# Kernel tuning notes

Hardware: AMD Instinct MI355X
Metric: run time of the kernel (lower is better)

Reference implementation:

```python
import jax, jax.numpy as jnp
import numpy as np

B, S, D = 16, 2048, 768
DOWNS = [16, 32, 64, 128]


def setup_inputs() -> dict:
    key = jax.random.key(0)
    ks = jax.random.split(key, 2 + 4 * len(DOWNS))
    inp = {
        "x": jax.random.normal(ks[0], (B, S, D), dtype=jnp.float32),
        "mask": jax.random.randint(ks[1], (B, S), 0, len(DOWNS), dtype=jnp.int64),
    }
    k = 2
    for i, ds in enumerate(DOWNS):
        inp[f"Wd{i}"] = jax.random.normal(ks[k], (D, ds), dtype=jnp.float32) * 0.02; k += 1
        inp[f"bd{i}"] = jax.random.normal(ks[k], (ds,), dtype=jnp.float32) * 0.02; k += 1
        inp[f"Wu{i}"] = jax.random.normal(ks[k], (ds, D), dtype=jnp.float32) * 0.02; k += 1
        inp[f"bu{i}"] = jax.random.normal(ks[k], (D,), dtype=jnp.float32) * 0.02; k += 1
    return inp


def reference(x, mask,
              Wd0, bd0, Wu0, bu0,
              Wd1, bd1, Wu1, bu1,
              Wd2, bd2, Wu2, bu2,
              Wd3, bd3, Wu3, bu3):
    # eval path, inference_level==0: all experts densely computed, then
    # per-token random mask selects one expert output (with residual) and sums.
    params = [(Wd0, bd0, Wu0, bu0), (Wd1, bd1, Wu1, bu1),
              (Wd2, bd2, Wu2, bu2), (Wd3, bd3, Wu3, bu3)]
    out = jnp.zeros_like(x)
    for i, (Wd, bd, Wu, bu) in enumerate(params):
        down = jax.nn.relu(jnp.einsum('bsd,dk->bsk', x, Wd) + bd)  # dropout is identity in eval
        up = jnp.einsum('bsk,kd->bsd', down, Wu) + bu + x          # residual add
        sel = (mask == i)[..., None].astype(x.dtype)               # [B,S,1]
        out = out + up * sel
    return out
```

## Files before the change

### kernel.cpp

```cpp
#include <hip/hip_runtime.h>
#include <hip/hip_bf16.h>

#define DIM 768
#define NTOK 32768
#define TTOK 16
#define NBLK 128

typedef __attribute__((ext_vector_type(8))) short short8;
typedef __attribute__((ext_vector_type(4))) float f32x4;

__device__ __forceinline__ unsigned short f2bf(float f) {
  union { float f; unsigned int u; } v; v.f = f;
  unsigned int u = v.u;
  return (unsigned short)((u + 0x7fffu + ((u >> 16) & 1u)) >> 16);
}
__device__ __forceinline__ float bf2f(unsigned short u) {
  union { unsigned int u; float f; } v; v.u = ((unsigned int)u) << 16; return v.f;
}

__global__ void hist_kernel(const int* __restrict__ mask, int* __restrict__ hist) {
  int tid = threadIdx.x, b = blockIdx.x;
  int gid = b * 256 + tid;
  int wv = tid >> 6, lane = tid & 63;
  int e = mask[gid] & 3;
  __shared__ int wcnt[4][4];
  #pragma unroll
  for (int q = 0; q < 4; ++q) {
    unsigned long long m = __ballot(e == q);
    if (lane == 0) wcnt[wv][q] = __popcll(m);
  }
  __syncthreads();
  if (tid < 4)
    hist[tid * NBLK + b] = wcnt[0][tid] + wcnt[1][tid] + wcnt[2][tid] + wcnt[3][tid];
}

__global__ void scan_kernel(const int* __restrict__ hist, int* __restrict__ base,
                            int* __restrict__ meta) {
  int lane = threadIdx.x;
  int v[8];
  int lsum = 0;
  #pragma unroll
  for (int j = 0; j < 8; ++j) {
    int t = hist[lane * 8 + j];
    v[j] = lsum; lsum += t;
  }
  int inc = lsum;
  #pragma unroll
  for (int d = 1; d < 64; d <<= 1) {
    int u = __shfl_up(inc, d);
    if (lane >= d) inc += u;
  }
  int excl = inc - lsum;
  #pragma unroll
  for (int j = 0; j < 8; ++j) base[lane * 8 + j] = excl + v[j];
  __syncthreads();
  if (lane == 0) {
    int est[5];
    #pragma unroll
    for (int e = 0; e < 4; ++e) est[e] = base[e * NBLK];
    est[4] = NTOK;
    #pragma unroll
    for (int e = 0; e < 5; ++e) meta[e] = est[e];
    int s = 0;
    #pragma unroll
    for (int e = 0; e < 4; ++e) {
      meta[8 + e] = s;
      s += (est[e + 1] - est[e] + TTOK - 1) / TTOK;
    }
    meta[12] = s;
    const int KPv[4] = {32, 32, 64, 128};
    int off = 0;
    #pragma unroll
    for (int e = 0; e < 4; ++e) {
      meta[16 + e] = off;
      int tiles = (est[e + 1] - est[e] + TTOK - 1) / TTOK;
      off += tiles * TTOK * KPv[e];
    }
  }
}

__global__ void scatter_kernel(const int* __restrict__ mask, const int* __restrict__ base,
                               int* __restrict__ lists) {
  int tid = threadIdx.x, b = blockIdx.x;
  int gid = b * 256 + tid;
  int wv = tid >> 6, lane = tid & 63;
  int e = mask[gid] & 3;
  __shared__ int wcnt[4][4];
  __shared__ int wbase[4][4];
  unsigned long long lt = (1ull << lane) - 1ull;
  int rank = 0;
  #pragma unroll
  for (int q = 0; q < 4; ++q) {
    unsigned long long m = __ballot(e == q);
    if (e == q) rank = __popcll(m & lt);
    if (lane == 0) wcnt[wv][q] = __popcll(m);
  }
  __syncthreads();
  if (tid < 4) {
    int s = 0;
    #pragma unroll
    for (int w2 = 0; w2 < 4; ++w2) { int c = wcnt[w2][tid]; wbase[w2][tid] = s; s += c; }
  }
  __syncthreads();
  lists[base[e * NBLK + b] + wbase[wv][e] + rank] = gid;
}

__global__ void prep_kernel(const float* __restrict__ Wd0, const float* __restrict__ Wd1,
                            const float* __restrict__ Wd2, const float* __restrict__ Wd3,
                            const float* __restrict__ Wu0, const float* __restrict__ Wu1,
                            const float* __restrict__ Wu2, const float* __restrict__ Wu3,
                            unsigned short* __restrict__ wdT, unsigned short* __restrict__ wuT) {
  int e = blockIdx.x;
  int ds = 16 << e;
  int lgK = (e == 0) ? 5 : (4 + e);
  int KP = 1 << lgK;
  const float* Wd = (e == 0) ? Wd0 : (e == 1) ? Wd1 : (e == 2) ? Wd2 : Wd3;
  const float* Wu = (e == 0) ? Wu0 : (e == 1) ? Wu1 : (e == 2) ? Wu2 : Wu3;
  const int WOFF[4] = {0, 12288, 36864, 86016};
  const int UOFF[4] = {0, 24576, 49152, 98304};
  int stride = gridDim.y * 256;
  int start = blockIdx.y * 256 + threadIdx.x;
  int nd = ds * DIM;
  for (int i = start; i < nd; i += stride) {
    int k = i / DIM, d = i - k * DIM;
    wdT[WOFF[e] + i] = f2bf(Wd[d * ds + k]);
  }
  int nu = DIM << lgK;
  for (int i = start; i < nu; i += stride) {
    int dc = i >> lgK, k = i & (KP - 1);
    wuT[UOFF[e] + i] = (k < ds) ? f2bf(Wu[k * DIM + dc]) : (unsigned short)0;
  }
}

__device__ __forceinline__ int expert_of(int w, const int* __restrict__ ts) {
  return (w >= ts[2]) ? ((w >= ts[3]) ? 3 : 2) : ((w >= ts[1]) ? 1 : 0);
}

template <int E>
__device__ __forceinline__ void down_tile(
    int wv, int lane, int tid, int tile, int cnt,
    const float* __restrict__ x, const int* __restrict__ listsE,
    const unsigned short* __restrict__ wd, const float* __restrict__ bd,
    unsigned short* __restrict__ dnE,
    unsigned short* __restrict__ xs, float* __restrict__ dnpart,
    unsigned short* __restrict__ dnt) {
  constexpr int DS = 16 << E;
  constexpr int KP = (E == 0) ? 32 : DS;
  constexpr int NTA = DS / 16;
  constexpr int SPLIT_N = (NTA < 4) ? NTA : 4;
  constexpr int SPLIT_K = 4 / SPLIT_N;
  constexpr int NTB = NTA / SPLIT_N;
  constexpr int KLEN = DIM / SPLIT_K;
  int base = tile * TTOK;
  int lrow = lane & 15, kg = lane >> 4;

  #pragma unroll
  for (int i = 0; i < 4; ++i) {
    int rr = base + wv * 4 + i;
    int t = (rr < cnt) ? listsE[rr] : -1;
    int r = wv * 4 + i;
    const float* src = x + (size_t)((t >= 0) ? t : 0) * DIM;
    #pragma unroll
    for (int j = 0; j < 3; ++j) {
      float4 v = {0.f, 0.f, 0.f, 0.f};
      if (t >= 0) v = *(const float4*)(src + j * 256 + lane * 4);
      ushort4 b;
      b.x = f2bf(v.x); b.y = f2bf(v.y); b.z = f2bf(v.z); b.w = f2bf(v.w);
      *(ushort4*)(xs + r * 776 + j * 256 + lane * 4) = b;
    }
  }
  if (SPLIT_K > 1) {
    for (int i = tid; i < TTOK * DS; i += 256) dnpart[i] = 0.f;
  }
  __syncthreads();

  int nsub = wv % SPLIT_N, ksub = wv / SPLIT_N;
  int d_base = ksub * KLEN;
  f32x4 acc[NTB];
  #pragma unroll
  for (int nb = 0; nb < NTB; ++nb) acc[nb] = f32x4{0.f, 0.f, 0.f, 0.f};

  for (int d0 = 0; d0 < KLEN; d0 += 64) {
    #pragma unroll
    for (int u = 0; u < 2; ++u) {
      int d = d_base + d0 + u * 32;
      short8 a = *(const short8*)(xs + lrow * 776 + d + kg * 8);
      #pragma unroll
      for (int nb = 0; nb < NTB; ++nb) {
        int n = nsub * NTB + nb;
        short8 b = *(const short8*)(wd + (size_t)(n * 16 + lrow) * DIM + d + kg * 8);
        acc[nb] = __builtin_amdgcn_mfma_f32_16x16x32_bf16(a, b, acc[nb], 0, 0, 0);
      }
    }
  }

  if (SPLIT_K > 1) {
    int kc = nsub * 16 + lrow;
    #pragma unroll
    for (int r = 0; r < 4; ++r)
      atomicAdd(&dnpart[(kg * 4 + r) * DS + kc], acc[0][r]);
    __syncthreads();
    for (int i = tid; i < TTOK * KP; i += 256) {
      int tt = i / KP, k = i - tt * KP;
      float v = (k < DS) ? fmaxf(dnpart[tt * DS + k] + bd[k], 0.f) : 0.f;
      dnt[tt * KP + k] = f2bf(v);
    }
  } else {
    #pragma unroll
    for (int nb = 0; nb < NTB; ++nb) {
      int kc = (nsub * NTB + nb) * 16 + lrow;
      float bv = bd[kc];
      #pragma unroll
      for (int r = 0; r < 4; ++r)
        dnt[(kg * 4 + r) * KP + kc] = f2bf(fmaxf(acc[nb][r] + bv, 0.f));
    }
  }
  __syncthreads();

  unsigned short* dst = dnE + (size_t)base * KP;
  constexpr int S = TTOK * KP;
  for (int i = tid * 8; i < S; i += 256 * 8)
    *(int4*)(dst + i) = *(const int4*)(dnt + i);
}

__global__ __launch_bounds__(256, 5) void down_main(
    const float* __restrict__ x,
    const int* __restrict__ meta, const int* __restrict__ lists,
    const unsigned short* __restrict__ wdT,
    const float* __restrict__ bd0, const float* __restrict__ bd1,
    const float* __restrict__ bd2, const float* __restrict__ bd3,
    unsigned short* __restrict__ dnc) {
  __shared__ unsigned short xs[TTOK * 776];
  __shared__ float dnpart[TTOK * 32];
  __shared__ unsigned short dnt[TTOK * 128];
  int tid = threadIdx.x, wv = tid >> 6, lane = tid & 63;
  const int* ts = meta + 8;
  int w = blockIdx.x;
  if (w >= ts[4]) return;
  int e = expert_of(w, ts);
  int tile = w - ts[e];
  int cnt = meta[e + 1] - meta[e];
  const int* listsE = lists + meta[e];
  const int WOFF[4] = {0, 12288, 36864, 86016};
  unsigned short* dnE = dnc + meta[16 + e];
  if (e == 0)
    down_tile<0>(wv, lane, tid, tile, cnt, x, listsE, wdT + WOFF[0], bd0, dnE, xs, dnpart, dnt);
  else if (e == 1)
    down_tile<1>(wv, lane, tid, tile, cnt, x, listsE, wdT + WOFF[1], bd1, dnE, xs, dnpart, dnt);
  else if (e == 2)
    down_tile<2>(wv, lane, tid, tile, cnt, x, listsE, wdT + WOFF[2], bd2, dnE, xs, dnpart, dnt);
  else
    down_tile<3>(wv, lane, tid, tile, cnt, x, listsE, wdT + WOFF[3], bd3, dnE, xs, dnpart, dnt);
}

template <int E>
__device__ __forceinline__ void up_tile(
    int wv, int lane, int tid, int tile, int cnt,
    const float* __restrict__ x, const int* __restrict__ listsE,
    const unsigned short* __restrict__ wu, const float* __restrict__ bu,
    const unsigned short* __restrict__ dnE, float* __restrict__ out,
    unsigned short* __restrict__ OL) {
  constexpr int DS = 16 << E;
  constexpr int KP = (E == 0) ? 32 : DS;
  constexpr int KB = KP / 32;
  int base = tile * TTOK;
  int lrow = lane & 15, kg = lane >> 4;

  short8 afr[KB];
  const unsigned short* dsrc = dnE + (size_t)(base + lrow) * KP + kg * 8;
  #pragma unroll
  for (int k = 0; k < KB; ++k) afr[k] = *(const short8*)(dsrc + k * 32);

  #pragma unroll 3
  for (int nn = 0; nn < 12; ++nn) {
    int n = wv * 12 + nn;
    f32x4 c = {0.f, 0.f, 0.f, 0.f};
    #pragma unroll
    for (int k = 0; k < KB; ++k) {
      short8 b = *(const short8*)(wu + (size_t)(n * 16 + lrow) * KP + k * 32 + kg * 8);
      c = __builtin_amdgcn_mfma_f32_16x16x32_bf16(afr[k], b, c, 0, 0, 0);
    }
    int dcol = n * 16 + lrow;
    float bv = bu[dcol];
    #pragma unroll
    for (int r = 0; r < 4; ++r)
      OL[(kg * 4 + r) * 772 + dcol] = f2bf(c[r] + bv);
  }
  __syncthreads();

  #pragma unroll
  for (int i = 0; i < 4; ++i) {
    int r = wv * 4 + i;
    int gr = base + r;
    int t = (gr < cnt) ? listsE[gr] : -1;
    if (t < 0) continue;
    const float* xsrc = x + (size_t)t * DIM;
    float* dst = out + (size_t)t * DIM;
    #pragma unroll
    for (int j = 0; j < 3; ++j) {
      int c4 = j * 256 + lane * 4;
      float4 xv = *(const float4*)(xsrc + c4);
      ushort4 ub = *(const ushort4*)(OL + r * 772 + c4);
      float4 o;
      o.x = xv.x + bf2f(ub.x);
      o.y = xv.y + bf2f(ub.y);
      o.z = xv.z + bf2f(ub.z);
      o.w = xv.w + bf2f(ub.w);
      *(float4*)(dst + c4) = o;
    }
  }
}

__global__ __launch_bounds__(256, 6) void up_main(
    const float* __restrict__ x,
    const int* __restrict__ meta, const int* __restrict__ lists,
    const unsigned short* __restrict__ wuT,
    const float* __restrict__ bu0, const float* __restrict__ bu1,
    const float* __restrict__ bu2, const float* __restrict__ bu3,
    const unsigned short* __restrict__ dnc, float* __restrict__ out) {
  __shared__ unsigned short OL[TTOK * 772];
  int tid = threadIdx.x, wv = tid >> 6, lane = tid & 63;
  const int* ts = meta + 8;
  int w = blockIdx.x;
  if (w >= ts[4]) return;
  int e = expert_of(w, ts);
  int tile = w - ts[e];
  int cnt = meta[e + 1] - meta[e];
  const int* listsE = lists + meta[e];
  const int UOFF[4] = {0, 24576, 49152, 98304};
  const unsigned short* dnE = dnc + meta[16 + e];
  if (e == 0)
    up_tile<0>(wv, lane, tid, tile, cnt, x, listsE, wuT + UOFF[0], bu0, dnE, out, OL);
  else if (e == 1)
    up_tile<1>(wv, lane, tid, tile, cnt, x, listsE, wuT + UOFF[1], bu1, dnE, out, OL);
  else if (e == 2)
    up_tile<2>(wv, lane, tid, tile, cnt, x, listsE, wuT + UOFF[2], bu2, dnE, out, OL);
  else
    up_tile<3>(wv, lane, tid, tile, cnt, x, listsE, wuT + UOFF[3], bu3, dnE, out, OL);
}

extern "C" void kernel_launch(void* const* d_in, const int* in_sizes, int n_in,
                              void* d_out, int out_size, void* d_ws, size_t ws_size,
                              hipStream_t stream) {
  const float* x = (const float*)d_in[0];
  const int* mask = (const int*)d_in[1];
  const float* Wd[4]; const float* bd[4]; const float* Wu[4]; const float* bu[4];
  for (int i = 0; i < 4; ++i) {
    Wd[i] = (const float*)d_in[2 + 4 * i];
    bd[i] = (const float*)d_in[3 + 4 * i];
    Wu[i] = (const float*)d_in[4 + 4 * i];
    bu[i] = (const float*)d_in[5 + 4 * i];
  }
  char* ws = (char*)d_ws;
  int* hist = (int*)ws;
  int* base = (int*)(ws + 2048);
  int* meta = (int*)(ws + 4096);
  int* lists = (int*)(ws + 4352);
  unsigned short* wdT = (unsigned short*)(ws + 135424);
  unsigned short* wuT = (unsigned short*)(ws + 504064);
  unsigned short* dnc = (unsigned short*)(ws + 897280);

  hist_kernel<<<NBLK, 256, 0, stream>>>(mask, hist);
  scan_kernel<<<1, 64, 0, stream>>>(hist, base, meta);
  scatter_kernel<<<NBLK, 256, 0, stream>>>(mask, base, lists);
  prep_kernel<<<dim3(4, 32), 256, 0, stream>>>(Wd[0], Wd[1], Wd[2], Wd[3],
                                               Wu[0], Wu[1], Wu[2], Wu[3], wdT, wuT);
  down_main<<<2051, 256, 0, stream>>>(x, meta, lists, wdT,
                                      bd[0], bd[1], bd[2], bd[3], dnc);
  up_main<<<2051, 256, 0, stream>>>(x, meta, lists, wuT,
                                    bu[0], bu[1], bu[2], bu[3], dnc,
                                    (float*)d_out);
}
```

Measured before the change: 116.0 us.

## Fuse down and up projections into persistent warp-specialized pipelined kernel

Replaces the separate down and up projection kernels with one persistent kernel of 512 blocks × 512 threads. Four waves gather x and run the down GEMM for tile i while the other four run the up GEMM and residual write for tile i-1, handing the intermediate activations through double-buffered shared memory. This removes the global round trip of the intermediate activations and one kernel launch, and overlaps the two stages. In exchange it adds extra block barriers per iteration, uses more LDS per block which may limit occupancy, and fixes the grid so some blocks may get one more tile than others.

Measured after the change: 100.8 us. -13.1%, faster.

```diff
diff --git a/kernel.cpp b/kernel.cpp
--- a/kernel.cpp
+++ b/kernel.cpp
@@ -5,6 +5,7 @@
 #define NTOK 32768
 #define TTOK 16
 #define NBLK 128
+#define GMAIN 512
 
 typedef __attribute__((ext_vector_type(8))) short short8;
 typedef __attribute__((ext_vector_type(4))) float f32x4;
@@ -68,14 +69,6 @@
       s += (est[e + 1] - est[e] + TTOK - 1) / TTOK;
     }
     meta[12] = s;
-    const int KPv[4] = {32, 32, 64, 128};
-    int off = 0;
-    #pragma unroll
-    for (int e = 0; e < 4; ++e) {
-      meta[16 + e] = off;
-      int tiles = (est[e + 1] - est[e] + TTOK - 1) / TTOK;
-      off += tiles * TTOK * KPv[e];
-    }
   }
 }
 
@@ -137,45 +130,21 @@
 }
 
 template <int E>
-__device__ __forceinline__ void down_tile(
-    int wv, int lane, int tid, int tile, int cnt,
-    const float* __restrict__ x, const int* __restrict__ listsE,
+__device__ __forceinline__ void down_g1(
+    int cwv, int lane,
     const unsigned short* __restrict__ wd, const float* __restrict__ bd,
-    unsigned short* __restrict__ dnE,
-    unsigned short* __restrict__ xs, float* __restrict__ dnpart,
-    unsigned short* __restrict__ dnt) {
+    const unsigned short* __restrict__ xs, float* __restrict__ dnpart,
+    unsigned short (*dnc)[136]) {
   constexpr int DS = 16 << E;
-  constexpr int KP = (E == 0) ? 32 : DS;
   constexpr int NTA = DS / 16;
   constexpr int SPLIT_N = (NTA < 4) ? NTA : 4;
   constexpr int SPLIT_K = 4 / SPLIT_N;
   constexpr int NTB = NTA / SPLIT_N;
   constexpr int KLEN = DIM / SPLIT_K;
-  int base = tile * TTOK;
   int lrow = lane & 15, kg = lane >> 4;
-
-  #pragma unroll
-  for (int i = 0; i < 4; ++i) {
-    int rr = base + wv * 4 + i;
-    int t = (rr < cnt) ? listsE[rr] : -1;
-    int r = wv * 4 + i;
-    const float* src = x + (size_t)((t >= 0) ? t : 0) * DIM;
-    #pragma unroll
-    for (int j = 0; j < 3; ++j) {
-      float4 v = {0.f, 0.f, 0.f, 0.f};
-      if (t >= 0) v = *(const float4*)(src + j * 256 + lane * 4);
-      ushort4 b;
-      b.x = f2bf(v.x); b.y = f2bf(v.y); b.z = f2bf(v.z); b.w = f2bf(v.w);
-      *(ushort4*)(xs + r * 776 + j * 256 + lane * 4) = b;
-    }
-  }
-  if (SPLIT_K > 1) {
-    for (int i = tid; i < TTOK * DS; i += 256) dnpart[i] = 0.f;
-  }
-  __syncthreads();
-
-  int nsub = wv % SPLIT_N, ksub = wv / SPLIT_N;
+  int nsub = cwv % SPLIT_N, ksub = cwv / SPLIT_N;
   int d_base = ksub * KLEN;
+
   f32x4 acc[NTB];
   #pragma unroll
   for (int nb = 0; nb < NTB; ++nb) acc[nb] = f32x4{0.f, 0.f, 0.f, 0.f};
@@ -199,12 +168,6 @@
     #pragma unroll
     for (int r = 0; r < 4; ++r)
       atomicAdd(&dnpart[(kg * 4 + r) * DS + kc], acc[0][r]);
-    __syncthreads();
-    for (int i = tid; i < TTOK * KP; i += 256) {
-      int tt = i / KP, k = i - tt * KP;
-      float v = (k < DS) ? fmaxf(dnpart[tt * DS + k] + bd[k], 0.f) : 0.f;
-      dnt[tt * KP + k] = f2bf(v);
-    }
   } else {
     #pragma unroll
     for (int nb = 0; nb < NTB; ++nb) {
@@ -212,68 +175,26 @@
       float bv = bd[kc];
       #pragma unroll
       for (int r = 0; r < 4; ++r)
-        dnt[(kg * 4 + r) * KP + kc] = f2bf(fmaxf(acc[nb][r] + bv, 0.f));
-    }
-  }
-  __syncthreads();
-
-  unsigned short* dst = dnE + (size_t)base * KP;
-  constexpr int S = TTOK * KP;
-  for (int i = tid * 8; i < S; i += 256 * 8)
-    *(int4*)(dst + i) = *(const int4*)(dnt + i);
-}
-
-__global__ __launch_bounds__(256, 5) void down_main(
-    const float* __restrict__ x,
-    const int* __restrict__ meta, const int* __restrict__ lists,
-    const unsigned short* __restrict__ wdT,
-    const float* __restrict__ bd0, const float* __restrict__ bd1,
-    const float* __restrict__ bd2, const float* __restrict__ bd3,
-    unsigned short* __restrict__ dnc) {
-  __shared__ unsigned short xs[TTOK * 776];
-  __shared__ float dnpart[TTOK * 32];
-  __shared__ unsigned short dnt[TTOK * 128];
-  int tid = threadIdx.x, wv = tid >> 6, lane = tid & 63;
-  const int* ts = meta + 8;
-  int w = blockIdx.x;
-  if (w >= ts[4]) return;
-  int e = expert_of(w, ts);
-  int tile = w - ts[e];
-  int cnt = meta[e + 1] - meta[e];
-  const int* listsE = lists + meta[e];
-  const int WOFF[4] = {0, 12288, 36864, 86016};
-  unsigned short* dnE = dnc + meta[16 + e];
-  if (e == 0)
-    down_tile<0>(wv, lane, tid, tile, cnt, x, listsE, wdT + WOFF[0], bd0, dnE, xs, dnpart, dnt);
-  else if (e == 1)
-    down_tile<1>(wv, lane, tid, tile, cnt, x, listsE, wdT + WOFF[1], bd1, dnE, xs, dnpart, dnt);
-  else if (e == 2)
-    down_tile<2>(wv, lane, tid, tile, cnt, x, listsE, wdT + WOFF[2], bd2, dnE, xs, dnpart, dnt);
-  else
-    down_tile<3>(wv, lane, tid, tile, cnt, x, listsE, wdT + WOFF[3], bd3, dnE, xs, dnpart, dnt);
+        dnc[kg * 4 + r][kc] = f2bf(fmaxf(acc[nb][r] + bv, 0.f));
+    }
+  }
 }
 
 template <int E>
-__device__ __forceinline__ void up_tile(
-    int wv, int lane, int tid, int tile, int cnt,
-    const float* __restrict__ x, const int* __restrict__ listsE,
+__device__ __forceinline__ void up_g2(
+    int cwv, int lane,
     const unsigned short* __restrict__ wu, const float* __restrict__ bu,
-    const unsigned short* __restrict__ dnE, float* __restrict__ out,
-    unsigned short* __restrict__ OL) {
-  constexpr int DS = 16 << E;
-  constexpr int KP = (E == 0) ? 32 : DS;
+    const unsigned short (*dnp)[136], unsigned short* __restrict__ OL) {
+  constexpr int KP = (E == 0) ? 32 : (16 << E);
   constexpr int KB = KP / 32;
-  int base = tile * TTOK;
   int lrow = lane & 15, kg = lane >> 4;
-
   short8 afr[KB];
-  const unsigned short* dsrc = dnE + (size_t)(base + lrow) * KP + kg * 8;
-  #pragma unroll
-  for (int k = 0; k < KB; ++k) afr[k] = *(const short8*)(dsrc + k * 32);
+  #pragma unroll
+  for (int k = 0; k < KB; ++k) afr[k] = *(const short8*)&dnp[lrow][k * 32 + kg * 8];
 
   #pragma unroll 3
   for (int nn = 0; nn < 12; ++nn) {
-    int n = wv * 12 + nn;
+    int n = cwv * 12 + nn;
     f32x4 c = {0.f, 0.f, 0.f, 0.f};
     #pragma unroll
     for (int k = 0; k < KB; ++k) {
@@ -286,57 +207,141 @@
     for (int r = 0; r < 4; ++r)
       OL[(kg * 4 + r) * 772 + dcol] = f2bf(c[r] + bv);
   }
-  __syncthreads();
-
-  #pragma unroll
-  for (int i = 0; i < 4; ++i) {
-    int r = wv * 4 + i;
-    int gr = base + r;
-    int t = (gr < cnt) ? listsE[gr] : -1;
-    if (t < 0) continue;
-    const float* xsrc = x + (size_t)t * DIM;
-    float* dst = out + (size_t)t * DIM;
-    #pragma unroll
-    for (int j = 0; j < 3; ++j) {
-      int c4 = j * 256 + lane * 4;
-      float4 xv = *(const float4*)(xsrc + c4);
-      ushort4 ub = *(const ushort4*)(OL + r * 772 + c4);
-      float4 o;
-      o.x = xv.x + bf2f(ub.x);
-      o.y = xv.y + bf2f(ub.y);
-      o.z = xv.z + bf2f(ub.z);
-      o.w = xv.w + bf2f(ub.w);
-      *(float4*)(dst + c4) = o;
-    }
-  }
-}
-
-__global__ __launch_bounds__(256, 6) void up_main(
+}
+
+__global__ __launch_bounds__(512, 4) void moe_main(
     const float* __restrict__ x,
     const int* __restrict__ meta, const int* __restrict__ lists,
-    const unsigned short* __restrict__ wuT,
+    const unsigned short* __restrict__ wdT, const unsigned short* __restrict__ wuT,
+    const float* __restrict__ bd0, const float* __restrict__ bd1,
+    const float* __restrict__ bd2, const float* __restrict__ bd3,
     const float* __restrict__ bu0, const float* __restrict__ bu1,
     const float* __restrict__ bu2, const float* __restrict__ bu3,
-    const unsigned short* __restrict__ dnc, float* __restrict__ out) {
+    float* __restrict__ out) {
+  __shared__ unsigned short xs[TTOK * 776];
+  __shared__ unsigned short dnb[2][TTOK][136];
+  __shared__ float dnpart[TTOK * 32];
   __shared__ unsigned short OL[TTOK * 772];
+  __shared__ int toksL[2][TTOK];
+
   int tid = threadIdx.x, wv = tid >> 6, lane = tid & 63;
+  bool dcrew = wv < 4;
+  int cwv = wv & 3;
+  int ctid = tid & 255;
   const int* ts = meta + 8;
-  int w = blockIdx.x;
-  if (w >= ts[4]) return;
-  int e = expert_of(w, ts);
-  int tile = w - ts[e];
-  int cnt = meta[e + 1] - meta[e];
-  const int* listsE = lists + meta[e];
+  int ntiles = ts[4];
+  int w0 = blockIdx.x;
+  if (w0 >= ntiles) return;
+  int ntb = (ntiles - 1 - w0) / GMAIN + 1;
+
+  if (dcrew) for (int i = ctid; i < TTOK * 32; i += 256) dnpart[i] = 0.f;
+
+  const int WOFF[4] = {0, 12288, 36864, 86016};
   const int UOFF[4] = {0, 24576, 49152, 98304};
-  const unsigned short* dnE = dnc + meta[16 + e];
-  if (e == 0)
-    up_tile<0>(wv, lane, tid, tile, cnt, x, listsE, wuT + UOFF[0], bu0, dnE, out, OL);
-  else if (e == 1)
-    up_tile<1>(wv, lane, tid, tile, cnt, x, listsE, wuT + UOFF[1], bu1, dnE, out, OL);
-  else if (e == 2)
-    up_tile<2>(wv, lane, tid, tile, cnt, x, listsE, wuT + UOFF[2], bu2, dnE, out, OL);
-  else
-    up_tile<3>(wv, lane, tid, tile, cnt, x, listsE, wuT + UOFF[3], bu3, dnE, out, OL);
+  const float* bds[4] = {bd0, bd1, bd2, bd3};
+  const float* bus[4] = {bu0, bu1, bu2, bu3};
+
+  for (int i = 0; i <= ntb; ++i) {
+    bool hasC = i < ntb, hasP = i > 0;
+    int cb = i & 1, pb = cb ^ 1;
+    int ec = 0, basec = 0, cntc = 0;
+    const int* listsC = lists;
+    if (hasC) {
+      int wc = w0 + i * GMAIN;
+      ec = expert_of(wc, ts);
+      basec = (wc - ts[ec]) * TTOK;
+      cntc = meta[ec + 1] - meta[ec];
+      listsC = lists + meta[ec];
+    }
+    int ep = 0;
+    if (hasP) ep = expert_of(w0 + (i - 1) * GMAIN, ts);
+    bool esplit = hasC && (ec <= 1);
+
+    if (dcrew) {
+      if (hasC) {
+        int myt[4];
+        #pragma unroll
+        for (int j = 0; j < 4; ++j) {
+          int r = basec + cwv * 4 + j;
+          myt[j] = (r < cntc) ? listsC[r] : -1;
+        }
+        if (ctid < TTOK)
+          toksL[cb][ctid] = (basec + ctid < cntc) ? listsC[basec + ctid] : -1;
+        #pragma unroll
+        for (int j = 0; j < 4; ++j) {
+          int r = cwv * 4 + j;
+          int t = myt[j];
+          const float* src = x + (size_t)((t >= 0) ? t : 0) * DIM;
+          #pragma unroll
+          for (int c = 0; c < 3; ++c) {
+            float4 v = {0.f, 0.f, 0.f, 0.f};
+            if (t >= 0) v = *(const float4*)(src + c * 256 + lane * 4);
+            ushort4 b;
+            b.x = f2bf(v.x); b.y = f2bf(v.y); b.z = f2bf(v.z); b.w = f2bf(v.w);
+            *(ushort4*)(xs + r * 776 + c * 256 + lane * 4) = b;
+          }
+        }
+      }
+    } else if (hasP) {
+      const unsigned short* wu = wuT + UOFF[ep];
+      const float* bu = bus[ep];
+      if (ep == 0)      up_g2<0>(cwv, lane, wu, bu, dnb[pb], OL);
+      else if (ep == 1) up_g2<1>(cwv, lane, wu, bu, dnb[pb], OL);
+      else if (ep == 2) up_g2<2>(cwv, lane, wu, bu, dnb[pb], OL);
+      else              up_g2<3>(cwv, lane, wu, bu, dnb[pb], OL);
+    }
+    __syncthreads();
+
+    if (dcrew) {
+      if (hasC) {
+        const unsigned short* wd = wdT + WOFF[ec];
+        const float* bd = bds[ec];
+        if (ec == 0)      down_g1<0>(cwv, lane, wd, bd, xs, dnpart, dnb[cb]);
+        else if (ec == 1) down_g1<1>(cwv, lane, wd, bd, xs, dnpart, dnb[cb]);
+        else if (ec == 2) down_g1<2>(cwv, lane, wd, bd, xs, dnpart, dnb[cb]);
+        else              down_g1<3>(cwv, lane, wd, bd, xs, dnpart, dnb[cb]);
+      }
+    } else if (hasP) {
+      #pragma unroll
+      for (int j = 0; j < 4; ++j) {
+        int r = cwv * 4 + j;
+        int t = toksL[pb][r];
+        if (t < 0) continue;
+        const float* xsrc = x + (size_t)t * DIM;
+        float* dst = out + (size_t)t * DIM;
+        #pragma unroll
+        for (int c = 0; c < 3; ++c) {
+          int c4 = c * 256 + lane * 4;
+          float4 xv = *(const float4*)(xsrc + c4);
+          ushort4 ub = *(const ushort4*)(OL + r * 772 + c4);
+          float4 o;
+          o.x = xv.x + bf2f(ub.x);
+          o.y = xv.y + bf2f(ub.y);
+          o.z = xv.z + bf2f(ub.z);
+          o.w = xv.w + bf2f(ub.w);
+          *(float4*)(dst + c4) = o;
+        }
+      }
+    }
+
+    if (esplit) {
+      __syncthreads();
+      if (dcrew) {
+        const float* bd = bds[ec];
+        int DS = (ec == 0) ? 16 : 32;
+        for (int ii = ctid; ii < TTOK * 32; ii += 256) {
+          int tt = ii >> 5, k = ii & 31;
+          float v = 0.f;
+          if (k < DS) {
+            v = fmaxf(dnpart[tt * DS + k] + bd[k], 0.f);
+            dnpart[tt * DS + k] = 0.f;
+          }
+          dnb[cb][tt][k] = f2bf(v);
+        }
+      }
+    }
+    __syncthreads();
+  }
 }
 
 extern "C" void kernel_launch(void* const* d_in, const int* in_sizes, int n_in,
@@ -358,16 +363,14 @@
   int* lists = (int*)(ws + 4352);
   unsigned short* wdT = (unsigned short*)(ws + 135424);
   unsigned short* wuT = (unsigned short*)(ws + 504064);
-  unsigned short* dnc = (unsigned short*)(ws + 897280);
 
   hist_kernel<<<NBLK, 256, 0, stream>>>(mask, hist);
   scan_kernel<<<1, 64, 0, stream>>>(hist, base, meta);
   scatter_kernel<<<NBLK, 256, 0, stream>>>(mask, base, lists);
   prep_kernel<<<dim3(4, 32), 256, 0, stream>>>(Wd[0], Wd[1], Wd[2], Wd[3],
                                                Wu[0], Wu[1], Wu[2], Wu[3], wdT, wuT);
-  down_main<<<2051, 256, 0, stream>>>(x, meta, lists, wdT,
-                                      bd[0], bd[1], bd[2], bd[3], dnc);
-  up_main<<<2051, 256, 0, stream>>>(x, meta, lists, wuT,
-                                    bu[0], bu[1], bu[2], bu[3], dnc,
-                                    (float*)d_out);
-}
+  moe_main<<<GMAIN, 512, 0, stream>>>(x, meta, lists, wdT, wuT,
+                                      bd[0], bd[1], bd[2], bd[3],
+                                      bu[0], bu[1], bu[2], bu[3],
+                                      (float*)d_out);
+}
```
